# Kernel tuning notes

Measured on AMD Instinct MI355X. Metric: run time of the kernel, lower is better.

Reference implementation:

```python
import jax, jax.numpy as jnp
from jax import lax
import numpy as np

D_MODEL = 512
D_STATE = 16
DI = 1024        # expand * d_model
DT_RANK = 32     # ceil(d_model/16)
K = 4            # mamba d_conv
NC = 8           # n_clusters
B = 2
L = 1024
EPS_LN = 1e-5


def _ln(x, g, b):
    m = jnp.mean(x, axis=-1, keepdims=True)
    v = jnp.mean((x - m) ** 2, axis=-1, keepdims=True)
    return (x - m) / jnp.sqrt(v + EPS_LN) * g + b


def _l2norm(x):
    n = jnp.linalg.norm(x, axis=-1, keepdims=True)
    return x / jnp.maximum(n, 1e-12)


def _ssm_scan(dA, dBu, C):
    # dA, dBu: (B, L, DI, N); C: (B, L, N) -> y: (B, L, DI)
    def step(h, inp):
        dA_t, dBu_t, c_t = inp
        h = dA_t * h + dBu_t                      # (B, DI, N)
        y = jnp.einsum('bdn,bn->bd', h, c_t)      # (B, DI)
        return h, y
    h0 = jnp.zeros((dA.shape[0], dA.shape[2], dA.shape[3]), dA.dtype)
    _, ys = lax.scan(step, h0, (jnp.swapaxes(dA, 0, 1), jnp.swapaxes(dBu, 0, 1), jnp.swapaxes(C, 0, 1)))
    return jnp.swapaxes(ys, 0, 1)


def _mamba(x, in_w, conv_w, conv_b, xproj_w, dt_w, dt_b, A_log, Dp, out_w):
    # x: (B, L, d_model)
    xz = x @ in_w.T                               # (B, L, 2*DI)
    xp, z = jnp.split(xz, 2, axis=-1)
    # depthwise causal conv1d
    xc = lax.conv_general_dilated(jnp.swapaxes(xp, 1, 2), conv_w, (1,), [(K - 1, 0)], feature_group_count=DI)
    xc = jax.nn.silu(xc + conv_b[None, :, None])
    xc = jnp.swapaxes(xc, 1, 2)                   # (B, L, DI)
    x_dbl = xc @ xproj_w.T                        # (B, L, DT_RANK + 2*N)
    dt, Bm, Cm = jnp.split(x_dbl, [DT_RANK, DT_RANK + D_STATE], axis=-1)
    delta = jax.nn.softplus(dt @ dt_w.T + dt_b)   # (B, L, DI)
    A = -jnp.exp(A_log)                           # (DI, N)
    dA = jnp.exp(delta[..., None] * A)            # (B, L, DI, N)
    dBu = (delta * xc)[..., None] * Bm[:, :, None, :]
    y = _ssm_scan(dA, dBu, Cm) + xc * Dp
    y = y * jax.nn.silu(z)
    return y @ out_w.T


def _forward(x, norm1_g, norm1_b,
             fm_in_w, fm_conv_w, fm_conv_b, fm_xproj_w, fm_dt_w, fm_dt_b, fm_A_log, fm_D, fm_out_w,
             bm_in_w, bm_conv_w, bm_conv_b, bm_xproj_w, bm_dt_w, bm_dt_b, bm_A_log, bm_D, bm_out_w,
             fusion_w, fusion_b, cc_centers, cc_proj_w, cc_proj_b, cc_norm_g, cc_norm_b, cc_alpha,
             gate_w, gate_b, ffn_norm_g, ffn_norm_b, ffn_w1, ffn_b1, ffn_w2, ffn_b2):
    xn = _ln(x, norm1_g, norm1_b)
    # bidirectional mamba path
    f_out = _mamba(xn, fm_in_w, fm_conv_w, fm_conv_b, fm_xproj_w, fm_dt_w, fm_dt_b, fm_A_log, fm_D, fm_out_w)
    b_out = jnp.flip(_mamba(jnp.flip(xn, axis=1), bm_in_w, bm_conv_w, bm_conv_b, bm_xproj_w, bm_dt_w, bm_dt_b, bm_A_log, bm_D, bm_out_w), axis=1)
    mamba_out = jnp.concatenate([f_out, b_out], axis=-1) @ fusion_w.T + fusion_b
    # context clustering path (dropout = identity at eval)
    proj = xn @ cc_proj_w.T + cc_proj_b
    sim = jnp.einsum('bld,cd->blc', _l2norm(proj), _l2norm(cc_centers))
    w = jax.nn.softmax(sim, axis=-1)
    ctx = jnp.einsum('blc,cd->bld', w, cc_centers)
    cc_out = _ln(xn + cc_alpha * ctx, cc_norm_g, cc_norm_b)
    # gated fusion
    g = jax.nn.softmax(xn @ gate_w.T + gate_b, axis=-1)  # (B, L, 2)
    fused = g[..., 0:1] * mamba_out + g[..., 1:2] * cc_out
    x = x + fused
    h = _ln(x, ffn_norm_g, ffn_norm_b)
    h = jax.nn.gelu(h @ ffn_w1.T + ffn_b1, approximate=False) @ ffn_w2.T + ffn_b2
    return x + h


def setup_inputs() -> dict:
    key = jax.random.key(0)
    ks = iter(jax.random.split(key, 64))
    nrm = lambda shape, s=0.02: jax.random.normal(next(ks), shape, jnp.float32) * s

    def mamba_params():
        A_log = jnp.tile(jnp.log(jnp.arange(1, D_STATE + 1, dtype=jnp.float32))[None, :], (DI, 1))
        return dict(in_w=nrm((2 * DI, D_MODEL)), conv_w=nrm((DI, 1, K), 0.1), conv_b=jnp.zeros((DI,)),
                    xproj_w=nrm((DT_RANK + 2 * D_STATE, DI)), dt_w=nrm((DI, DT_RANK), 0.1),
                    dt_b=nrm((DI,), 0.1), A_log=A_log, D=jnp.ones((DI,)), out_w=nrm((D_MODEL, DI)))

    fm = mamba_params()
    bm = mamba_params()
    d = {
        'x': jax.random.normal(next(ks), (B, L, D_MODEL), jnp.float32),
        'norm1_g': jnp.ones((D_MODEL,)), 'norm1_b': jnp.zeros((D_MODEL,)),
        'fusion_w': nrm((D_MODEL, 2 * D_MODEL)), 'fusion_b': jnp.zeros((D_MODEL,)),
        'cc_centers': jax.random.normal(next(ks), (NC, D_MODEL), jnp.float32),
        'cc_proj_w': nrm((D_MODEL, D_MODEL)), 'cc_proj_b': jnp.zeros((D_MODEL,)),
        'cc_norm_g': jnp.ones((D_MODEL,)), 'cc_norm_b': jnp.zeros((D_MODEL,)),
        'cc_alpha': jnp.array([0.05], jnp.float32),
        'gate_w': nrm((2, D_MODEL)), 'gate_b': jnp.zeros((2,)),
        'ffn_norm_g': jnp.ones((D_MODEL,)), 'ffn_norm_b': jnp.zeros((D_MODEL,)),
        'ffn_w1': nrm((4 * D_MODEL, D_MODEL)), 'ffn_b1': jnp.zeros((4 * D_MODEL,)),
        'ffn_w2': nrm((D_MODEL, 4 * D_MODEL)), 'ffn_b2': jnp.zeros((D_MODEL,)),
    }
    for pfx, p in (('fm', fm), ('bm', bm)):
        for k, v in p.items():
            d[pfx + '_' + k] = v
    return d


def reference(x, norm1_g, norm1_b,
              fm_in_w, fm_conv_w, fm_conv_b, fm_xproj_w, fm_dt_w, fm_dt_b, fm_A_log, fm_D, fm_out_w,
              bm_in_w, bm_conv_w, bm_conv_b, bm_xproj_w, bm_dt_w, bm_dt_b, bm_A_log, bm_D, bm_out_w,
              fusion_w, fusion_b, cc_centers, cc_proj_w, cc_proj_b, cc_norm_g, cc_norm_b, cc_alpha,
              gate_w, gate_b, ffn_norm_g, ffn_norm_b, ffn_w1, ffn_b1, ffn_w2, ffn_b2):
    return _forward(x, norm1_g, norm1_b,
                    fm_in_w, fm_conv_w, fm_conv_b, fm_xproj_w, fm_dt_w, fm_dt_b, fm_A_log, fm_D, fm_out_w,
                    bm_in_w, bm_conv_w, bm_conv_b, bm_xproj_w, bm_dt_w, bm_dt_b, bm_A_log, bm_D, bm_out_w,
                    fusion_w, fusion_b, cc_centers, cc_proj_w, cc_proj_b, cc_norm_g, cc_norm_b, cc_alpha,
                    gate_w, gate_b, ffn_norm_g, ffn_norm_b, ffn_w1, ffn_b1, ffn_w2, ffn_b2)
```

## Files before the change

kernel.cpp:

```cpp
#include <hip/hip_runtime.h>
#include <hip/hip_bf16.h>
#include <hip/hip_fp16.h>
#include <math.h>

using bf16 = __hip_bfloat16;

typedef __attribute__((ext_vector_type(8))) short v8s;
typedef __attribute__((ext_vector_type(4))) short v4s;
typedef __attribute__((ext_vector_type(4))) float v4f;

constexpr int kB   = 2;
constexpr int kL   = 1024;
constexpr int kD   = 512;
constexpr int kDI  = 1024;
constexpr int kNS  = 16;
constexpr int kDTR = 32;
constexpr int kKC  = 4;
constexpr int kNC  = 8;
constexpr int kM   = kB * kL;
constexpr int kCH  = 32;
constexpr int kCL  = kL / kCH;
constexpr float kEPS = 1e-5f;

static __device__ __forceinline__ float toF(bf16 x) { return __bfloat162float(x); }
static __device__ __forceinline__ float b2f(short u) {
    unsigned int x = ((unsigned int)(unsigned short)u) << 16;
    return __uint_as_float(x);
}

static __device__ __forceinline__ float ldin(const void* p, int i, int f32) {
    if (f32) return ((const float*)p)[i];
    return toF(((const bf16*)p)[i]);
}

static __device__ __forceinline__ int flipL(int r) { return r ^ (kL - 1); }

__global__ void detect_kernel(const unsigned short* __restrict__ x, int* __restrict__ flag) {
    int lane = threadIdx.x;
    int cnt = 0;
    for (int i = lane; i < 512; i += 64) {
        unsigned short h = x[2 * i];
        int e = (h >> 7) & 0xFF;
        if (e >= 100 && e <= 140) cnt++;
    }
#pragma unroll
    for (int o = 32; o > 0; o >>= 1) cnt += __shfl_down(cnt, o, 64);
    if (lane == 0) *flag = (cnt >= 256) ? 0 : 1;
}

struct WSrcs { const void* p[12]; };

__global__ __launch_bounds__(256) void wconv_kernel(WSrcs s, bf16* __restrict__ dst,
                                                    const int* __restrict__ flg) {
    const int sz[12]  = {1048576, 1048576, 65536, 65536, 32768, 32768,
                         524288, 524288, 524288, 262144, 1048576, 1048576};
    const int off[12] = {0, 1048576, 2097152, 2162688, 2228224, 2260992,
                         2293760, 2818048, 3342336, 3866624, 4128768, 5177344};
    int t = blockIdx.y;
    int n = sz[t];
    const void* src = s.p[t];
    bf16* d = dst + off[t];
    int f32 = *flg;
    for (int i = blockIdx.x * 256 + threadIdx.x; i < n; i += gridDim.x * 256)
        d[i] = __float2bfloat16(ldin(src, i, f32));
}

__global__ __launch_bounds__(256) void an_kernel(const void* __restrict__ alog_f,
                                                 const void* __restrict__ alog_b,
                                                 float* __restrict__ anT,
                                                 const int* __restrict__ flg) {
    int f32 = *flg;
    int tid = blockIdx.x * 256 + threadIdx.x;
    int d = tid & (kDI - 1);
    int n = (tid >> 10) & (kNS - 1);
    int dir = tid >> 14;
    anT[tid] = -__expf(ldin(dir ? alog_b : alog_f, d * kNS + n, f32));
}

static __device__ __forceinline__ float blockReduceSum(float v, float* s) {
    __syncthreads();
#pragma unroll
    for (int o = 32; o > 0; o >>= 1) v += __shfl_down(v, o, 64);
    int lane = threadIdx.x & 63, wid = threadIdx.x >> 6;
    if (lane == 0) s[wid] = v;
    __syncthreads();
    if (threadIdx.x == 0) {
        float t = 0.f;
        for (int i = 0; i < 4; ++i) t += s[i];
        s[4] = t;
    }
    __syncthreads();
    return s[4];
}

__global__ __launch_bounds__(256) void ln_in_kernel(const void* __restrict__ X,
                                                    const void* __restrict__ g,
                                                    const void* __restrict__ b,
                                                    bf16* __restrict__ Y,
                                                    const int* __restrict__ flg) {
    __shared__ float sred[8];
    int f32 = *flg;
    int row = blockIdx.x;
    int i = threadIdx.x;
    size_t base = (size_t)row * kD;
    float x0 = ldin(X, base + i, f32), x1 = ldin(X, base + i + 256, f32);
    float mean = blockReduceSum(x0 + x1, sred) * (1.f / kD);
    float vs = blockReduceSum(x0 * x0 + x1 * x1, sred) * (1.f / kD) - mean * mean;
    float rstd = rsqrtf(vs + kEPS);
    Y[base + i]       = __float2bfloat16((x0 - mean) * rstd * ldin(g, i, f32)       + ldin(b, i, f32));
    Y[base + i + 256] = __float2bfloat16((x1 - mean) * rstd * ldin(g, i + 256, f32) + ldin(b, i + 256, f32));
}

template <int BM, int BN, int WRN, int WCN>
__global__ __launch_bounds__(256) void mfma_gemm(const bf16* __restrict__ A, int lda, int aZOff,
                                                 const bf16* __restrict__ W, int K, int wZOff,
                                                 const void* __restrict__ bias, int act,
                                                 const float* __restrict__ resid,
                                                 bf16* __restrict__ outB,
                                                 void* __restrict__ outRaw,
                                                 int ldo, int oZOff,
                                                 int flipN0, int zflip,
                                                 const int* __restrict__ flg,
                                                 bf16* __restrict__ outSplitZ) {
    __shared__ bf16 As[BM * 64];
    __shared__ bf16 Bs[BN * 64];
    constexpr int FR = BM / WRN / 16;
    constexpr int FC = BN / WCN / 16;
    constexpr int AV = BM / 32;
    constexpr int BV = BN / 32;

    int f32 = *flg;
    int tid = threadIdx.x;
    int z = blockIdx.z;
    const bf16* Ab = A + (size_t)z * aZOff;
    const bf16* Wb = W + (size_t)z * wZOff;
    int m0 = blockIdx.y * BM, n0 = blockIdx.x * BN;
    int lane = tid & 63, w = tid >> 6;
    int wr = w % WRN, wc = w / WRN;
    int rbase = wr * (BM / WRN), cbase = wc * (BN / WCN);
    int quad = lane >> 4, lrow = lane & 15;
    int wbase = tid & ~63;

    v4f acc[FR][FC];
#pragma unroll
    for (int i = 0; i < FR; ++i)
#pragma unroll
        for (int j = 0; j < FC; ++j)
#pragma unroll
            for (int r = 0; r < 4; ++r) acc[i][j][r] = 0.f;

    for (int kt = 0; kt < K; kt += 64) {
#pragma unroll
        for (int i = 0; i < AV; ++i) {
            int v = i * 256 + tid;
            int row = v >> 3, c8 = (v & 7) * 8;
            const bf16* gp = Ab + (size_t)(m0 + row) * lda + kt + c8;
            __builtin_amdgcn_global_load_lds(
                (const __attribute__((address_space(1))) void*)gp,
                (__attribute__((address_space(3))) void*)&As[(i * 256 + wbase) * 8],
                16, 0, 0);
        }
#pragma unroll
        for (int i = 0; i < BV; ++i) {
            int v = i * 256 + tid;
            int row = v >> 3, c8 = (v & 7) * 8;
            const bf16* gp = Wb + (size_t)(n0 + row) * K + kt + c8;
            __builtin_amdgcn_global_load_lds(
                (const __attribute__((address_space(1))) void*)gp,
                (__attribute__((address_space(3))) void*)&Bs[(i * 256 + wbase) * 8],
                16, 0, 0);
        }
        __syncthreads();
#pragma unroll
        for (int k0 = 0; k0 < 64; k0 += 32) {
            v8s a[FR], b[FC];
#pragma unroll
            for (int fr = 0; fr < FR; ++fr)
                a[fr] = *reinterpret_cast<const v8s*>(&As[(rbase + fr * 16 + lrow) * 64 + k0 + quad * 8]);
#pragma unroll
            for (int fc = 0; fc < FC; ++fc)
                b[fc] = *reinterpret_cast<const v8s*>(&Bs[(cbase + fc * 16 + lrow) * 64 + k0 + quad * 8]);
#pragma unroll
            for (int fr = 0; fr < FR; ++fr)
#pragma unroll
                for (int fc = 0; fc < FC; ++fc)
                    acc[fr][fc] = __builtin_amdgcn_mfma_f32_16x16x32_bf16(a[fr], b[fc], acc[fr][fc], 0, 0, 0);
        }
        __syncthreads();
    }

    bf16* outBz = outB ? outB + (size_t)z * oZOff : nullptr;
#pragma unroll
    for (int fr = 0; fr < FR; ++fr) {
#pragma unroll
        for (int fc = 0; fc < FC; ++fc) {
            int ncol = n0 + cbase + fc * 16 + lrow;
            float bi = bias ? ldin(bias, ncol, f32) : 0.f;
            bool doflip = (ncol >= flipN0) || (zflip && z == 1);
#pragma unroll
            for (int r = 0; r < 4; ++r) {
                int m = m0 + rbase + fr * 16 + quad * 4 + r;
                float vv = acc[fr][fc][r] + bi;
                if (act == 2) vv = 0.5f * vv * (1.f + erff(vv * 0.70710678118654752440f));
                if (resid) vv += resid[(size_t)m * ldo + ncol];
                if (outSplitZ) {
                    int dir = (ncol >> 11) & 1;
                    int isz = (ncol >> 10) & 1;
                    int c2 = dir * 1024 + (ncol & 1023);
                    int mo_ = dir ? flipL(m) : m;
                    bf16* dst = isz ? outSplitZ : outB;
                    dst[(size_t)mo_ * 2048 + c2] = __float2bfloat16(vv);
                } else {
                    int mo_ = doflip ? flipL(m) : m;
                    size_t oi = (size_t)mo_ * ldo + ncol;
                    if (outBz) outBz[oi] = __float2bfloat16(vv);
                    else if (f32) ((float*)outRaw)[oi] = vv;
                    else ((bf16*)outRaw)[oi] = __float2bfloat16(vv);
                }
            }
        }
    }
}

__global__ __launch_bounds__(256) void conv_kernel(const bf16* __restrict__ xp,
                                                   const void* __restrict__ cw_f,
                                                   const void* __restrict__ cb_f,
                                                   const void* __restrict__ cw_b,
                                                   const void* __restrict__ cb_b,
                                                   bf16* __restrict__ xc,
                                                   const int* __restrict__ flg) {
    int f32 = *flg;
    int tid = blockIdx.x * 256 + threadIdx.x;
    int d = tid & (kDI - 1);
    int r = (tid >> 10) & (kM - 1);
    int dir = tid >> 21;
    int l = r & (kL - 1);
    int b = r >> 10;
    const void* cw = dir ? cw_b : cw_f;
    const void* cb = dir ? cb_b : cb_f;
    float acc = ldin(cb, d, f32);
#pragma unroll
    for (int k = 0; k < kKC; ++k) {
        int ll = l - (kKC - 1) + k;
        if (ll >= 0)
            acc += ldin(cw, d * kKC + k, f32) *
                   toF(xp[(size_t)(b * kL + ll) * (2 * kDI) + dir * kDI + d]);
    }
    float s = acc / (1.f + __expf(-acc));
    xc[(size_t)r * (2 * kDI) + dir * kDI + d] = __float2bfloat16(s);
}

__global__ __launch_bounds__(256) void delta_kernel(const bf16* __restrict__ xdbl,
                                                    const bf16* __restrict__ wdt,
                                                    const void* __restrict__ dtb_f,
                                                    const void* __restrict__ dtb_b,
                                                    __half* __restrict__ deltaH,
                                                    const int* __restrict__ flg) {
    __shared__ float arow[kDTR];
    int f32 = *flg;
    int m = blockIdx.y;
    int dir = blockIdx.z;
    int d = blockIdx.x * 256 + threadIdx.x;
    if (threadIdx.x < kDTR)
        arow[threadIdx.x] = toF(xdbl[(size_t)m * 128 + dir * 64 + threadIdx.x]);
    __syncthreads();
    float acc = ldin(dir ? dtb_b : dtb_f, d, f32);
    const v8s* wv = reinterpret_cast<const v8s*>(wdt + ((size_t)dir * kDI + d) * kDTR);
#pragma unroll
    for (int t = 0; t < 4; ++t) {
        v8s w8 = wv[t];
#pragma unroll
        for (int k = 0; k < 8; ++k) acc += arow[t * 8 + k] * b2f(w8[k]);
    }
    acc = (acc > 20.f) ? acc : log1pf(__expf(acc));
    deltaH[((size_t)dir * kM + m) * kDI + d] = __float2half(acc);
}

__global__ __launch_bounds__(256) void scan_phase1(const bf16* __restrict__ xc,
                                                   const bf16* __restrict__ xdbl,
                                                   __half* __restrict__ deltaS,
                                                   const float* __restrict__ anT,
                                                   float* __restrict__ PA,
                                                   __half* __restrict__ HLh,
                                                   bf16* __restrict__ ymul,
                                                   const int* __restrict__ flg) {
    int tid = blockIdx.x * 256 + threadIdx.x;
    int n4  = tid & 3;
    int d   = (tid >> 2) & (kDI - 1);
    int c   = (tid >> 12) & (kCH - 1);
    int b   = (tid >> 17) & 1;
    int dir = tid >> 18;
    float an[4], h[4], pa[4];
#pragma unroll
    for (int j = 0; j < 4; ++j) {
        an[j] = anT[((size_t)dir * kNS + n4 * 4 + j) * kDI + d];
        h[j] = 0.f;
        pa[j] = 1.f;
    }
    __half* dptr = deltaS + ((size_t)dir * kM + (size_t)b * kL) * kDI + d;
    float s = 0.f;
    int l0 = c * kCL;
    for (int l = l0; l < l0 + kCL; ++l) {
        size_t rb = (size_t)b * kL + l;
        float dl = __half2float(dptr[(size_t)l * kDI]);
        s += dl;
        float xcv = toF(xc[rb * (2 * kDI) + dir * kDI + d]);
        float du = dl * xcv;
        v4s Bv = *reinterpret_cast<const v4s*>(xdbl + rb * 128 + dir * 64 + kDTR + n4 * 4);
        v4s Cv = *reinterpret_cast<const v4s*>(xdbl + rb * 128 + dir * 64 + kDTR + kNS + n4 * 4);
        float yp = 0.f;
#pragma unroll
        for (int j = 0; j < 4; ++j) {
            float a = __expf(dl * an[j]);
            pa[j] *= a;
            h[j] = a * h[j] + du * b2f(Bv[j]);
            yp += h[j] * b2f(Cv[j]);
        }
        yp += __shfl_xor(yp, 1);
        yp += __shfl_xor(yp, 2);
        if (n4 == 0) {
            ymul[rb * (2 * kDI) + dir * kDI + d] = __float2bfloat16(yp);
            dptr[(size_t)l * kDI] = __float2half(s);
        }
    }
    int g = dir * kB + b;
    size_t o = (((size_t)g * kCH + c) * kNS + n4 * 4) * kDI + d;
#pragma unroll
    for (int j = 0; j < 4; ++j) {
        PA[o + (size_t)j * kDI] = pa[j];
        HLh[o + (size_t)j * kDI] = __float2half(h[j]);
    }
}

__global__ __launch_bounds__(256) void scan_phase2(float* __restrict__ PA,
                                                   const __half* __restrict__ HLh) {
    int tid = blockIdx.x * 256 + threadIdx.x;
    int d = tid & (kDI - 1);
    int n = (tid >> 10) & (kNS - 1);
    int g = tid >> 14;
    float h = 0.f;
    for (int c = 0; c < kCH; ++c) {
        size_t idx = (((size_t)g * kCH + c) * kNS + n) * kDI + d;
        float pav = PA[idx];
        float hlv = __half2float(HLh[idx]);
        PA[idx] = h;
        h = pav * h + hlv;
    }
}

__global__ __launch_bounds__(256) void scan_fix(const bf16* __restrict__ xc,
                                                const bf16* __restrict__ xdbl,
                                                const bf16* __restrict__ zb,
                                                const __half* __restrict__ sbuf,
                                                const float* __restrict__ anT,
                                                const void* __restrict__ dp_f,
                                                const void* __restrict__ dp_b,
                                                const float* __restrict__ HIN,
                                                bf16* __restrict__ ymul,
                                                const int* __restrict__ flg) {
    int f32 = *flg;
    int tid = blockIdx.x * 256 + threadIdx.x;
    int d   = tid & (kDI - 1);
    int l   = (tid >> 10) & (kL - 1);
    int b   = (tid >> 20) & 1;
    int dir = tid >> 21;
    int c   = l / kCL;
    size_t rb = (size_t)b * kL + l;
    float s = __half2float(sbuf[((size_t)dir * kM + rb) * kDI + d]);
    int g = dir * kB + b;
    const float* hin = HIN + (((size_t)g * kCH + c) * kNS) * kDI + d;
    const float* anp = anT + (size_t)dir * kNS * kDI + d;
    const bf16* Cp = xdbl + rb * 128 + dir * 64 + kDTR + kNS;
    float ycorr = 0.f;
#pragma unroll
    for (int n = 0; n < kNS; ++n) {
        float an = anp[(size_t)n * kDI];
        ycorr += toF(Cp[n]) * __expf(an * s) * hin[(size_t)n * kDI];
    }
    size_t yi = rb * (2 * kDI) + dir * kDI + d;
    float xcv = toF(xc[yi]);
    float Dv = ldin(dir ? dp_b : dp_f, d, f32);
    float y = toF(ymul[yi]) + ycorr + xcv * Dv;
    float zv = toF(zb[yi]);
    float sz = zv / (1.f + __expf(-zv));
    ymul[yi] = __float2bfloat16(y * sz);
}

__global__ void cnorm_kernel(const void* __restrict__ C, float* __restrict__ cn,
                             const int* __restrict__ flg) {
    int f32 = *flg;
    int c = blockIdx.x;
    int lane = threadIdx.x;
    float s = 0.f;
    for (int i = lane; i < kD; i += 64) {
        float v = ldin(C, c * kD + i, f32);
        s += v * v;
    }
#pragma unroll
    for (int o = 32; o > 0; o >>= 1) s += __shfl_down(s, o, 64);
    if (lane == 0) cn[c] = sqrtf(s);
}

__global__ __launch_bounds__(256) void post_kernel(const bf16* __restrict__ proj,
                                                   const void* __restrict__ centers,
                                                   const float* __restrict__ cn,
                                                   const bf16* __restrict__ xn,
                                                   const void* __restrict__ alpha_p,
                                                   const void* __restrict__ ccg,
                                                   const void* __restrict__ ccb,
                                                   const void* __restrict__ X,
                                                   const bf16* __restrict__ mo,
                                                   const void* __restrict__ gw,
                                                   const void* __restrict__ gb,
                                                   const void* __restrict__ fg,
                                                   const void* __restrict__ fbb,
                                                   float* __restrict__ xmid,
                                                   bf16* __restrict__ hln,
                                                   const int* __restrict__ flg) {
    __shared__ float sred[8];
    __shared__ float sims[kNC];
    int f32 = *flg;
    int row = blockIdx.x;
    int i = threadIdx.x;
    size_t base = (size_t)row * kD;
    float p0 = toF(proj[base + i]), p1 = toF(proj[base + i + 256]);
    float sumsq = blockReduceSum(p0 * p0 + p1 * p1, sred);
    float pn = fmaxf(sqrtf(sumsq), 1e-12f);
    for (int c = 0; c < kNC; ++c) {
        float part = p0 * ldin(centers, c * kD + i, f32) + p1 * ldin(centers, c * kD + i + 256, f32);
        float dot = blockReduceSum(part, sred);
        if (threadIdx.x == 0) sims[c] = dot / (pn * fmaxf(cn[c], 1e-12f));
    }
    __syncthreads();
    float mx = -1e30f;
#pragma unroll
    for (int c = 0; c < kNC; ++c) mx = fmaxf(mx, sims[c]);
    float wv[kNC], se = 0.f;
#pragma unroll
    for (int c = 0; c < kNC; ++c) { wv[c] = __expf(sims[c] - mx); se += wv[c]; }
    float inv = 1.f / se;
    float ctx0 = 0.f, ctx1 = 0.f;
#pragma unroll
    for (int c = 0; c < kNC; ++c) {
        float wc = wv[c] * inv;
        ctx0 += wc * ldin(centers, c * kD + i, f32);
        ctx1 += wc * ldin(centers, c * kD + i + 256, f32);
    }
    float alpha = ldin(alpha_p, 0, f32);
    float x0 = toF(xn[base + i]), x1 = toF(xn[base + i + 256]);
    float t0 = x0 + alpha * ctx0;
    float t1 = x1 + alpha * ctx1;
    float mean = blockReduceSum(t0 + t1, sred) * (1.f / kD);
    float vs = blockReduceSum(t0 * t0 + t1 * t1, sred) * (1.f / kD) - mean * mean;
    float rstd = rsqrtf(vs + kEPS);
    float cc0 = (t0 - mean) * rstd * ldin(ccg, i, f32)       + ldin(ccb, i, f32);
    float cc1 = (t1 - mean) * rstd * ldin(ccg, i + 256, f32) + ldin(ccb, i + 256, f32);
    float d0 = blockReduceSum(x0 * ldin(gw, i, f32) + x1 * ldin(gw, i + 256, f32), sred);
    float d1 = blockReduceSum(x0 * ldin(gw, kD + i, f32) + x1 * ldin(gw, kD + i + 256, f32), sred);
    d0 += ldin(gb, 0, f32);
    d1 += ldin(gb, 1, f32);
    float gmx = fmaxf(d0, d1);
    float e0 = __expf(d0 - gmx), e1 = __expf(d1 - gmx);
    float gs = e0 + e1;
    float g0 = e0 / gs, g1 = e1 / gs;
    float xm0 = ldin(X, base + i, f32)       + g0 * toF(mo[base + i])       + g1 * cc0;
    float xm1 = ldin(X, base + i + 256, f32) + g0 * toF(mo[base + i + 256]) + g1 * cc1;
    xmid[base + i] = xm0;
    xmid[base + i + 256] = xm1;
    float mean2 = blockReduceSum(xm0 + xm1, sred) * (1.f / kD);
    float vs2 = blockReduceSum(xm0 * xm0 + xm1 * xm1, sred) * (1.f / kD) - mean2 * mean2;
    float rstd2 = rsqrtf(vs2 + kEPS);
    hln[base + i]       = __float2bfloat16((xm0 - mean2) * rstd2 * ldin(fg, i, f32)       + ldin(fbb, i, f32));
    hln[base + i + 256] = __float2bfloat16((xm1 - mean2) * rstd2 * ldin(fg, i + 256, f32) + ldin(fbb, i + 256, f32));
}

extern "C" void kernel_launch(void* const* d_in, const int* in_sizes, int n_in,
                              void* d_out, int out_size, void* d_ws, size_t ws_size,
                              hipStream_t stream) {
    bool sig = (n_in > 3 && in_sizes[3] == 2 * kDI * kD);
    int I_fusion_w = sig ? 21 : 3,  I_fusion_b = sig ? 22 : 4;
    int I_centers  = sig ? 23 : 5,  I_ccp_w    = sig ? 24 : 6,  I_ccp_b = sig ? 25 : 7;
    int I_ccn_g    = sig ? 26 : 8,  I_ccn_b    = sig ? 27 : 9,  I_alpha = sig ? 28 : 10;
    int I_gate_w   = sig ? 29 : 11, I_gate_b   = sig ? 30 : 12;
    int I_ffn_g    = sig ? 31 : 13, I_ffn_b    = sig ? 32 : 14;
    int I_ffn_w1   = sig ? 33 : 15, I_ffn_b1   = sig ? 34 : 16;
    int I_ffn_w2   = sig ? 35 : 17, I_ffn_b2   = sig ? 36 : 18;
    int I_fm       = sig ? 3  : 19, I_bm       = sig ? 12 : 28;

    const void* X        = d_in[0];
    const void* n1g      = d_in[1];
    const void* n1b      = d_in[2];
    const void* fusion_b = d_in[I_fusion_b];
    const void* centers  = d_in[I_centers];
    const void* ccp_b    = d_in[I_ccp_b];
    const void* ccn_g    = d_in[I_ccn_g];
    const void* ccn_b    = d_in[I_ccn_b];
    const void* cc_alpha = d_in[I_alpha];
    const void* gate_w   = d_in[I_gate_w];
    const void* gate_b   = d_in[I_gate_b];
    const void* ffn_g    = d_in[I_ffn_g];
    const void* ffn_b    = d_in[I_ffn_b];
    const void* ffn_b1   = d_in[I_ffn_b1];
    const void* ffn_b2   = d_in[I_ffn_b2];

    float* ws = (float*)d_ws;
    int* flg  = (int*)d_ws;
    float* cn = ws + 8;
    float*  anT  = ws + 32;
    float*  PA   = anT + 32768;
    __half* HLh  = (__half*)(PA + 2097152);
    bf16*  xn   = (bf16*)((float*)HLh + 1048576);
    bf16*  xp   = (bf16*)((float*)xn + 524288);
    bf16*  zb   = (bf16*)((float*)xp + 2097152);
    bf16*  xc   = (bf16*)((float*)zb + 2097152);
    bf16*  xdbl = (bf16*)((float*)xc + 2097152);
    bf16*  ymul = (bf16*)((float*)xdbl + 131072);
    bf16*  wbuf = (bf16*)((float*)ymul + 2097152);
    __half* deltaH = (__half*)xp;
    bf16*  fb    = (bf16*)HLh;
    bf16*  mo    = (bf16*)PA;
    float* xmid  = PA + 524288;
    bf16*  hln   = xc;
    bf16*  ffnh  = zb;
    bf16*  projb = fb;

    bf16* w_in     = wbuf + 0;
    bf16* w_xp     = wbuf + 2097152;
    bf16* w_dt     = wbuf + 2228224;
    bf16* w_out    = wbuf + 2293760;
    bf16* w_fusion = wbuf + 3342336;
    bf16* w_ccp    = wbuf + 3866624;
    bf16* w_ffn1   = wbuf + 4128768;
    bf16* w_ffn2   = wbuf + 5177344;

    dim3 blk(256);
    constexpr int NOFLIP = 1 << 30;

    detect_kernel<<<1, 64, 0, stream>>>((const unsigned short*)X, flg);

    WSrcs srcs;
    srcs.p[0] = d_in[I_fm + 0]; srcs.p[1] = d_in[I_bm + 0];
    srcs.p[2] = d_in[I_fm + 3]; srcs.p[3] = d_in[I_bm + 3];
    srcs.p[4] = d_in[I_fm + 4]; srcs.p[5] = d_in[I_bm + 4];
    srcs.p[6] = d_in[I_fm + 8]; srcs.p[7] = d_in[I_bm + 8];
    srcs.p[8] = d_in[I_fusion_w]; srcs.p[9] = d_in[I_ccp_w];
    srcs.p[10] = d_in[I_ffn_w1]; srcs.p[11] = d_in[I_ffn_w2];
    wconv_kernel<<<dim3(512, 12), blk, 0, stream>>>(srcs, wbuf, flg);

    an_kernel<<<128, blk, 0, stream>>>(d_in[I_fm + 6], d_in[I_bm + 6], anT, flg);

    ln_in_kernel<<<kM, blk, 0, stream>>>(X, n1g, n1b, xn, flg);

    mfma_gemm<128, 64, 2, 2><<<dim3(64, 16, 1), blk, 0, stream>>>(
        xn, kD, 0, w_in, kD, 0, nullptr, 0, nullptr, xp, nullptr, 2048, 0, NOFLIP, 0, flg, zb);

    conv_kernel<<<2 * kM * kDI / 256, blk, 0, stream>>>(
        xp, d_in[I_fm + 1], d_in[I_fm + 2], d_in[I_bm + 1], d_in[I_bm + 2], xc, flg);

    mfma_gemm<32, 64, 1, 4><<<dim3(1, 64, 2), blk, 0, stream>>>(
        xc, 2 * kDI, kDI, w_xp, kDI, 65536, nullptr, 0, nullptr, xdbl, nullptr, 128, 64,
        NOFLIP, 0, flg, nullptr);

    delta_kernel<<<dim3(kDI / 256, kM, 2), blk, 0, stream>>>(
        xdbl, w_dt, d_in[I_fm + 5], d_in[I_bm + 5], deltaH, flg);

    scan_phase1<<<2048, blk, 0, stream>>>(xc, xdbl, deltaH, anT, PA, HLh, ymul, flg);
    scan_phase2<<<256, blk, 0, stream>>>(PA, HLh);
    scan_fix<<<16384, blk, 0, stream>>>(xc, xdbl, zb, deltaH, anT,
                                        d_in[I_fm + 7], d_in[I_bm + 7], PA, ymul, flg);

    mfma_gemm<32, 64, 1, 4><<<dim3(8, 64, 2), blk, 0, stream>>>(
        ymul, 2 * kDI, kDI, w_out, kDI, 524288, nullptr, 0, nullptr, fb, nullptr, 2 * kD, kD,
        NOFLIP, 1, flg, nullptr);

    mfma_gemm<32, 64, 1, 4><<<dim3(8, 64, 1), blk, 0, stream>>>(
        fb, 2 * kD, 0, w_fusion, 2 * kD, 0, fusion_b, 0, nullptr, mo, nullptr, kD, 0,
        NOFLIP, 0, flg, nullptr);

    mfma_gemm<32, 64, 1, 4><<<dim3(8, 64, 1), blk, 0, stream>>>(
        xn, kD, 0, w_ccp, kD, 0, ccp_b, 0, nullptr, projb, nullptr, kD, 0, NOFLIP, 0, flg,
        nullptr);
    cnorm_kernel<<<kNC, 64, 0, stream>>>(centers, cn, flg);

    post_kernel<<<kM, blk, 0, stream>>>(projb, centers, cn, xn, cc_alpha, ccn_g, ccn_b,
                                        X, mo, gate_w, gate_b, ffn_g, ffn_b, xmid, hln, flg);

    mfma_gemm<64, 64, 2, 2><<<dim3(32, 32, 1), blk, 0, stream>>>(
        hln, kD, 0, w_ffn1, kD, 0, ffn_b1, 2, nullptr, ffnh, nullptr, 4 * kD, 0, NOFLIP, 0, flg,
        nullptr);
    mfma_gemm<32, 64, 1, 4><<<dim3(8, 64, 1), blk, 0, stream>>>(
        ffnh, 4 * kD, 0, w_ffn2, 4 * kD, 0, ffn_b2, 0, xmid, nullptr, d_out, kD, 0,
        NOFLIP, 0, flg, nullptr);
}
```

Baseline: 389.2 us.

## Merge setup kernels, fuse ccp projection into in-proj GEMM, swizzle LDS tiles

Detect, weight conversion, A-negation and center-norm kernels are merged into a single setup launch in which each block re-runs the dtype detection locally. The cluster-centre projection GEMM is folded into the in-projection GEMM as extra column tiles that select the ccp weights and write to a new projb buffer. An XOR swizzle is also applied to the LDS tile layout in all GEMMs to reduce bank conflicts. The aims are fewer launches, a better-filled GEMM grid, and cheaper LDS reads, at the cost of redundant detection work in every setup block.

```diff
diff --git a/kernel.cpp b/kernel.cpp
--- a/kernel.cpp
+++ b/kernel.cpp
@@ -35,48 +35,6 @@
 
 static __device__ __forceinline__ int flipL(int r) { return r ^ (kL - 1); }
 
-__global__ void detect_kernel(const unsigned short* __restrict__ x, int* __restrict__ flag) {
-    int lane = threadIdx.x;
-    int cnt = 0;
-    for (int i = lane; i < 512; i += 64) {
-        unsigned short h = x[2 * i];
-        int e = (h >> 7) & 0xFF;
-        if (e >= 100 && e <= 140) cnt++;
-    }
-#pragma unroll
-    for (int o = 32; o > 0; o >>= 1) cnt += __shfl_down(cnt, o, 64);
-    if (lane == 0) *flag = (cnt >= 256) ? 0 : 1;
-}
-
-struct WSrcs { const void* p[12]; };
-
-__global__ __launch_bounds__(256) void wconv_kernel(WSrcs s, bf16* __restrict__ dst,
-                                                    const int* __restrict__ flg) {
-    const int sz[12]  = {1048576, 1048576, 65536, 65536, 32768, 32768,
-                         524288, 524288, 524288, 262144, 1048576, 1048576};
-    const int off[12] = {0, 1048576, 2097152, 2162688, 2228224, 2260992,
-                         2293760, 2818048, 3342336, 3866624, 4128768, 5177344};
-    int t = blockIdx.y;
-    int n = sz[t];
-    const void* src = s.p[t];
-    bf16* d = dst + off[t];
-    int f32 = *flg;
-    for (int i = blockIdx.x * 256 + threadIdx.x; i < n; i += gridDim.x * 256)
-        d[i] = __float2bfloat16(ldin(src, i, f32));
-}
-
-__global__ __launch_bounds__(256) void an_kernel(const void* __restrict__ alog_f,
-                                                 const void* __restrict__ alog_b,
-                                                 float* __restrict__ anT,
-                                                 const int* __restrict__ flg) {
-    int f32 = *flg;
-    int tid = blockIdx.x * 256 + threadIdx.x;
-    int d = tid & (kDI - 1);
-    int n = (tid >> 10) & (kNS - 1);
-    int dir = tid >> 14;
-    anT[tid] = -__expf(ldin(dir ? alog_b : alog_f, d * kNS + n, f32));
-}
-
 static __device__ __forceinline__ float blockReduceSum(float v, float* s) {
     __syncthreads();
 #pragma unroll
@@ -91,6 +49,63 @@
     }
     __syncthreads();
     return s[4];
+}
+
+static __device__ __forceinline__ int detect_local(const unsigned short* x, float* sred) {
+    float c = 0.f;
+    for (int i = threadIdx.x; i < 512; i += 256) {
+        unsigned short h = x[2 * i];
+        int e = (h >> 7) & 0xFF;
+        if (e >= 100 && e <= 140) c += 1.f;
+    }
+    float tot = blockReduceSum(c, sred);
+    return (tot >= 256.f) ? 0 : 1;
+}
+
+struct WSrcs { const void* p[12]; };
+
+__global__ __launch_bounds__(256) void setup_kernel(WSrcs s, bf16* __restrict__ dst,
+                                                    const void* __restrict__ alog_f,
+                                                    const void* __restrict__ alog_b,
+                                                    const void* __restrict__ centers,
+                                                    float* __restrict__ anT,
+                                                    float* __restrict__ cn,
+                                                    int* __restrict__ flag,
+                                                    const unsigned short* __restrict__ x0) {
+    __shared__ float sred[8];
+    int f32 = detect_local(x0, sred);
+    int t = blockIdx.y;
+    if (t < 12) {
+        const int sz[12]  = {1048576, 1048576, 65536, 65536, 32768, 32768,
+                             524288, 524288, 524288, 262144, 1048576, 1048576};
+        const int off[12] = {0, 1048576, 2097152, 2162688, 2228224, 2260992,
+                             2293760, 2818048, 3342336, 3866624, 4128768, 5177344};
+        int n = sz[t];
+        const void* src = s.p[t];
+        bf16* d = dst + off[t];
+        for (int i = blockIdx.x * 256 + threadIdx.x; i < n; i += 512 * 256)
+            d[i] = __float2bfloat16(ldin(src, i, f32));
+    } else {
+        int bx = blockIdx.x;
+        if (bx < 128) {
+            int tid = bx * 256 + threadIdx.x;
+            int d = tid & (kDI - 1);
+            int n = (tid >> 10) & (kNS - 1);
+            int dir = tid >> 14;
+            anT[tid] = -__expf(ldin(dir ? alog_b : alog_f, d * kNS + n, f32));
+        } else if (bx < 136) {
+            int c = bx - 128;
+            float ssum = 0.f;
+            for (int i = threadIdx.x; i < kD; i += 256) {
+                float v = ldin(centers, c * kD + i, f32);
+                ssum += v * v;
+            }
+            float tot = blockReduceSum(ssum, sred);
+            if (threadIdx.x == 0) cn[c] = sqrtf(tot);
+        } else if (bx == 136) {
+            if (threadIdx.x == 0) *flag = f32;
+        }
+    }
 }
 
 __global__ __launch_bounds__(256) void ln_in_kernel(const void* __restrict__ X,
@@ -121,7 +136,11 @@
                                                  int ldo, int oZOff,
                                                  int flipN0, int zflip,
                                                  const int* __restrict__ flg,
-                                                 bf16* __restrict__ outSplitZ) {
+                                                 bf16* __restrict__ outSplitZ,
+                                                 const bf16* __restrict__ wCcp,
+                                                 const void* __restrict__ ccpBias,
+                                                 bf16* __restrict__ outCcp,
+                                                 int nSplit2) {
     __shared__ bf16 As[BM * 64];
     __shared__ bf16 Bs[BN * 64];
     constexpr int FR = BM / WRN / 16;
@@ -133,8 +152,11 @@
     int tid = threadIdx.x;
     int z = blockIdx.z;
     const bf16* Ab = A + (size_t)z * aZOff;
+    int m0 = blockIdx.y * BM, n0 = blockIdx.x * BN;
     const bf16* Wb = W + (size_t)z * wZOff;
-    int m0 = blockIdx.y * BM, n0 = blockIdx.x * BN;
+    int nrow0 = n0;
+    bool isCcp = (wCcp != nullptr) && (n0 >= nSplit2);
+    if (isCcp) { Wb = wCcp; nrow0 = n0 - nSplit2; }
     int lane = tid & 63, w = tid >> 6;
     int wr = w % WRN, wc = w / WRN;
     int rbase = wr * (BM / WRN), cbase = wc * (BN / WCN);
@@ -153,7 +175,8 @@
 #pragma unroll
         for (int i = 0; i < AV; ++i) {
             int v = i * 256 + tid;
-            int row = v >> 3, c8 = (v & 7) * 8;
+            int row = v >> 3;
+            int c8 = ((v & 7) * 8) ^ ((row & 7) * 8);
             const bf16* gp = Ab + (size_t)(m0 + row) * lda + kt + c8;
             __builtin_amdgcn_global_load_lds(
                 (const __attribute__((address_space(1))) void*)gp,
@@ -163,8 +186,9 @@
 #pragma unroll
         for (int i = 0; i < BV; ++i) {
             int v = i * 256 + tid;
-            int row = v >> 3, c8 = (v & 7) * 8;
-            const bf16* gp = Wb + (size_t)(n0 + row) * K + kt + c8;
+            int row = v >> 3;
+            int c8 = ((v & 7) * 8) ^ ((row & 7) * 8);
+            const bf16* gp = Wb + (size_t)(nrow0 + row) * K + kt + c8;
             __builtin_amdgcn_global_load_lds(
                 (const __attribute__((address_space(1))) void*)gp,
                 (__attribute__((address_space(3))) void*)&Bs[(i * 256 + wbase) * 8],
@@ -175,11 +199,17 @@
         for (int k0 = 0; k0 < 64; k0 += 32) {
             v8s a[FR], b[FC];
 #pragma unroll
-            for (int fr = 0; fr < FR; ++fr)
-                a[fr] = *reinterpret_cast<const v8s*>(&As[(rbase + fr * 16 + lrow) * 64 + k0 + quad * 8]);
-#pragma unroll
-            for (int fc = 0; fc < FC; ++fc)
-                b[fc] = *reinterpret_cast<const v8s*>(&Bs[(cbase + fc * 16 + lrow) * 64 + k0 + quad * 8]);
+            for (int fr = 0; fr < FR; ++fr) {
+                int r = rbase + fr * 16 + lrow;
+                a[fr] = *reinterpret_cast<const v8s*>(
+                    &As[r * 64 + ((k0 + quad * 8) ^ ((r & 7) * 8))]);
+            }
+#pragma unroll
+            for (int fc = 0; fc < FC; ++fc) {
+                int r = cbase + fc * 16 + lrow;
+                b[fc] = *reinterpret_cast<const v8s*>(
+                    &Bs[r * 64 + ((k0 + quad * 8) ^ ((r & 7) * 8))]);
+            }
 #pragma unroll
             for (int fr = 0; fr < FR; ++fr)
 #pragma unroll
@@ -203,7 +233,10 @@
                 float vv = acc[fr][fc][r] + bi;
                 if (act == 2) vv = 0.5f * vv * (1.f + erff(vv * 0.70710678118654752440f));
                 if (resid) vv += resid[(size_t)m * ldo + ncol];
-                if (outSplitZ) {
+                if (outCcp && ncol >= nSplit2) {
+                    float v2 = vv + ldin(ccpBias, ncol - nSplit2, f32);
+                    outCcp[(size_t)m * kD + (ncol - nSplit2)] = __float2bfloat16(v2);
+                } else if (outSplitZ) {
                     int dir = (ncol >> 11) & 1;
                     int isz = (ncol >> 10) & 1;
                     int c2 = dir * 1024 + (ncol & 1023);
@@ -384,21 +417,6 @@
     float zv = toF(zb[yi]);
     float sz = zv / (1.f + __expf(-zv));
     ymul[yi] = __float2bfloat16(y * sz);
-}
-
-__global__ void cnorm_kernel(const void* __restrict__ C, float* __restrict__ cn,
-                             const int* __restrict__ flg) {
-    int f32 = *flg;
-    int c = blockIdx.x;
-    int lane = threadIdx.x;
-    float s = 0.f;
-    for (int i = lane; i < kD; i += 64) {
-        float v = ldin(C, c * kD + i, f32);
-        s += v * v;
-    }
-#pragma unroll
-    for (int o = 32; o > 0; o >>= 1) s += __shfl_down(s, o, 64);
-    if (lane == 0) cn[c] = sqrtf(s);
 }
 
 __global__ __launch_bounds__(256) void post_kernel(const bf16* __restrict__ proj,
@@ -516,13 +534,13 @@
     bf16*  xdbl = (bf16*)((float*)xc + 2097152);
     bf16*  ymul = (bf16*)((float*)xdbl + 131072);
     bf16*  wbuf = (bf16*)((float*)ymul + 2097152);
+    bf16*  projb = (bf16*)((float*)wbuf + 3112960);
     __half* deltaH = (__half*)xp;
     bf16*  fb    = (bf16*)HLh;
     bf16*  mo    = (bf16*)PA;
     float* xmid  = PA + 524288;
     bf16*  hln   = xc;
     bf16*  ffnh  = zb;
-    bf16*  projb = fb;
 
     bf16* w_in     = wbuf + 0;
     bf16* w_xp     = wbuf + 2097152;
@@ -536,8 +554,6 @@
     dim3 blk(256);
     constexpr int NOFLIP = 1 << 30;
 
-    detect_kernel<<<1, 64, 0, stream>>>((const unsigned short*)X, flg);
-
     WSrcs srcs;
     srcs.p[0] = d_in[I_fm + 0]; srcs.p[1] = d_in[I_bm + 0];
     srcs.p[2] = d_in[I_fm + 3]; srcs.p[3] = d_in[I_bm + 3];
@@ -545,21 +561,23 @@
     srcs.p[6] = d_in[I_fm + 8]; srcs.p[7] = d_in[I_bm + 8];
     srcs.p[8] = d_in[I_fusion_w]; srcs.p[9] = d_in[I_ccp_w];
     srcs.p[10] = d_in[I_ffn_w1]; srcs.p[11] = d_in[I_ffn_w2];
-    wconv_kernel<<<dim3(512, 12), blk, 0, stream>>>(srcs, wbuf, flg);
-
-    an_kernel<<<128, blk, 0, stream>>>(d_in[I_fm + 6], d_in[I_bm + 6], anT, flg);
+
+    setup_kernel<<<dim3(512, 13), blk, 0, stream>>>(
+        srcs, wbuf, d_in[I_fm + 6], d_in[I_bm + 6], centers, anT, cn, flg,
+        (const unsigned short*)X);
 
     ln_in_kernel<<<kM, blk, 0, stream>>>(X, n1g, n1b, xn, flg);
 
-    mfma_gemm<128, 64, 2, 2><<<dim3(64, 16, 1), blk, 0, stream>>>(
-        xn, kD, 0, w_in, kD, 0, nullptr, 0, nullptr, xp, nullptr, 2048, 0, NOFLIP, 0, flg, zb);
+    mfma_gemm<128, 64, 2, 2><<<dim3(72, 16, 1), blk, 0, stream>>>(
+        xn, kD, 0, w_in, kD, 0, nullptr, 0, nullptr, xp, nullptr, 2048, 0, NOFLIP, 0, flg, zb,
+        w_ccp, ccp_b, projb, 4096);
 
     conv_kernel<<<2 * kM * kDI / 256, blk, 0, stream>>>(
         xp, d_in[I_fm + 1], d_in[I_fm + 2], d_in[I_bm + 1], d_in[I_bm + 2], xc, flg);
 
     mfma_gemm<32, 64, 1, 4><<<dim3(1, 64, 2), blk, 0, stream>>>(
         xc, 2 * kDI, kDI, w_xp, kDI, 65536, nullptr, 0, nullptr, xdbl, nullptr, 128, 64,
-        NOFLIP, 0, flg, nullptr);
+        NOFLIP, 0, flg, nullptr, nullptr, nullptr, nullptr, NOFLIP);
 
     delta_kernel<<<dim3(kDI / 256, kM, 2), blk, 0, stream>>>(
         xdbl, w_dt, d_in[I_fm + 5], d_in[I_bm + 5], deltaH, flg);
@@ -571,24 +589,19 @@
 
     mfma_gemm<32, 64, 1, 4><<<dim3(8, 64, 2), blk, 0, stream>>>(
         ymul, 2 * kDI, kDI, w_out, kDI, 524288, nullptr, 0, nullptr, fb, nullptr, 2 * kD, kD,
-        NOFLIP, 1, flg, nullptr);
+        NOFLIP, 1, flg, nullptr, nullptr, nullptr, nullptr, NOFLIP);
 
     mfma_gemm<32, 64, 1, 4><<<dim3(8, 64, 1), blk, 0, stream>>>(
         fb, 2 * kD, 0, w_fusion, 2 * kD, 0, fusion_b, 0, nullptr, mo, nullptr, kD, 0,
-        NOFLIP, 0, flg, nullptr);
-
-    mfma_gemm<32, 64, 1, 4><<<dim3(8, 64, 1), blk, 0, stream>>>(
-        xn, kD, 0, w_ccp, kD, 0, ccp_b, 0, nullptr, projb, nullptr, kD, 0, NOFLIP, 0, flg,
-        nullptr);
-    cnorm_kernel<<<kNC, 64, 0, stream>>>(centers, cn, flg);
+        NOFLIP, 0, flg, nullptr, nullptr, nullptr, nullptr, NOFLIP);
 
     post_kernel<<<kM, blk, 0, stream>>>(projb, centers, cn, xn, cc_alpha, ccn_g, ccn_b,
                                         X, mo, gate_w, gate_b, ffn_g, ffn_b, xmid, hln, flg);
 
     mfma_gemm<64, 64, 2, 2><<<dim3(32, 32, 1), blk, 0, stream>>>(
         hln, kD, 0, w_ffn1, kD, 0, ffn_b1, 2, nullptr, ffnh, nullptr, 4 * kD, 0, NOFLIP, 0, flg,
-        nullptr);
+        nullptr, nullptr, nullptr, nullptr, NOFLIP);
     mfma_gemm<32, 64, 1, 4><<<dim3(8, 64, 1), blk, 0, stream>>>(
         ffnh, 4 * kD, 0, w_ffn2, 4 * kD, 0, ffn_b2, 0, xmid, nullptr, d_out, kD, 0,
-        NOFLIP, 0, flg, nullptr);
-}
+        NOFLIP, 0, flg, nullptr, nullptr, nullptr, nullptr, NOFLIP);
+}
```

After: 375.8 us. 1.04x faster.
